# Kernel optimization log

Measured on AMD Instinct MI355X. Metric: run time of the kernel, lower is better.

The kernel has to match this reference:

```python
import jax, jax.numpy as jnp
import numpy as np

EMBED_DIM = 1024
NUM_HEADS = 16
HEAD_DIM = EMBED_DIM // NUM_HEADS
EPSILON = 0.01
C = 2.0 + EPSILON
SCORE_SCALE = 1.0
B, L = 2, 2048


def setup_inputs() -> dict:
    key = jax.random.key(0)
    k0, k1, k2, k3, k4 = jax.random.split(key, 5)
    x = jax.random.normal(k0, (B, L, EMBED_DIM), dtype=jnp.float32)
    # flax Linear kernels: (in, out)
    W_qkv = jax.random.normal(k1, (EMBED_DIM, 3 * EMBED_DIM), dtype=jnp.float32) / np.sqrt(EMBED_DIM)
    b_qkv = jnp.zeros((3 * EMBED_DIM,), dtype=jnp.float32)
    W_out = jax.random.normal(k2, (EMBED_DIM, EMBED_DIM), dtype=jnp.float32) / np.sqrt(EMBED_DIM)
    b_out = jnp.zeros((EMBED_DIM,), dtype=jnp.float32)
    return {"x": x, "W_qkv": W_qkv, "b_qkv": b_qkv, "W_out": W_out, "b_out": b_out}


def reference(x, W_qkv, b_qkv, W_out, b_out):
    Bb, Ll, E = x.shape
    qkv = x @ W_qkv + b_qkv                      # [B, L, 3E]
    q, k, v = jnp.split(qkv, 3, axis=-1)
    def to_heads(t):
        return t.reshape(Bb, Ll, NUM_HEADS, HEAD_DIM).transpose(0, 2, 1, 3)  # [B,H,L,D]
    q, k, v = to_heads(q), to_heads(k), to_heads(v)
    q_norm = q / jnp.linalg.norm(q, axis=-1, keepdims=True)
    k_norm = k / jnp.linalg.norm(k, axis=-1, keepdims=True)
    x_dot = jnp.einsum('bhid,bhjd->bhij', q_norm, k_norm)   # [B,H,L,L]
    scores = (x_dot ** 2) / (C - 2.0 * x_dot) * SCORE_SCALE
    mask = jnp.triu(jnp.ones((Ll, Ll), dtype=scores.dtype), k=1) * -1e9
    scores = scores + mask[None, None, :, :]
    attn = jax.nn.softmax(scores, axis=-1)
    out = jnp.einsum('bhij,bhjd->bhid', attn, v)            # [B,H,L,D]
    out = out.transpose(0, 2, 1, 3).reshape(Bb, Ll, E)
    return out @ W_out + b_out
```

## Files before the change

### kernel.cpp

```cpp
#include <hip/hip_runtime.h>
#include <cstdint>
#include <cstddef>

#define B_DIM 2
#define L_DIM 2048
#define E_DIM 1024
#define H_DIM 16
#define HD    64
#define M_ROWS (B_DIM * L_DIM)
#define QKV_N  (3 * E_DIM)
#define C_CONST 2.01f
#define NCH_BH 80
#define LOG2E 1.4426950408889634f
#define LN2   0.6931471805599453f

typedef unsigned short ushort_t;
typedef __attribute__((ext_vector_type(8))) short bf16x8;
typedef __attribute__((ext_vector_type(4))) float f32x4;

__device__ __forceinline__ unsigned int f2bf(float f) {
    union { float f; unsigned int u; } v; v.f = f;
    return (v.u + 0x7FFFu + ((v.u >> 16) & 1u)) >> 16;
}
__device__ __forceinline__ float bf2f_lo(unsigned int u) {
    union { unsigned int u; float f; } v; v.u = u << 16; return v.f;
}
__device__ __forceinline__ float bf2f_hi(unsigned int u) {
    union { unsigned int u; float f; } v; v.u = u & 0xffff0000u; return v.f;
}

__device__ __forceinline__ void gload16(const void* g, void* l) {
    __builtin_amdgcn_global_load_lds(
        (const __attribute__((address_space(1))) void*)g,
        (__attribute__((address_space(3))) void*)l, 16, 0, 0);
}

__global__ __launch_bounds__(256) void cast_bf16_kernel(
    const float* __restrict__ in, ushort_t* __restrict__ out, int n4)
{
    const int i = blockIdx.x * 256 + threadIdx.x;
    if (i >= n4) return;
    const float4 v = ((const float4*)in)[i];
    uint2 p;
    p.x = f2bf(v.x) | (f2bf(v.y) << 16);
    p.y = f2bf(v.z) | (f2bf(v.w) << 16);
    ((uint2*)out)[i] = p;
}

__global__ __launch_bounds__(256) void transpose_bf16_kernel(
    const float* __restrict__ in, ushort_t* __restrict__ out, int R, int Cn)
{
    __shared__ float t[64][65];
    const int c0 = blockIdx.x * 64, r0 = blockIdx.y * 64;
    const int tid = threadIdx.x;
    for (int idx = tid; idx < 4096; idx += 256) {
        const int r = idx >> 6, c = idx & 63;
        t[r][c] = in[(size_t)(r0 + r) * Cn + c0 + c];
    }
    __syncthreads();
    for (int idx = tid; idx < 4096; idx += 256) {
        const int c = idx >> 6, r = idx & 63;
        out[(size_t)(c0 + c) * R + r0 + r] = (ushort_t)f2bf(t[r][c]);
    }
}

template<int NCOLS, int MODE>
__global__ __launch_bounds__(256) void gemm_bt_kernel(
    const ushort_t* __restrict__ A, const ushort_t* __restrict__ BT,
    const float* __restrict__ bias, float* __restrict__ outf,
    ushort_t* __restrict__ q16, ushort_t* __restrict__ k16,
    ushort_t* __restrict__ v16)
{
    __shared__ __align__(16) ushort_t Abuf[128 * 32];
    __shared__ __align__(16) ushort_t Bbuf[128 * 32];
    const int tid = threadIdx.x;
    const int wave = tid >> 6, lane = tid & 63;
    const int m0 = blockIdx.x * 128, n0 = blockIdx.y * 128;
    const int wr = (wave >> 1) * 64, wc = (wave & 1) * 64;
    const int g = lane >> 4, l15 = lane & 15;

    f32x4 acc[4][4];
    #pragma unroll
    for (int i = 0; i < 4; ++i)
        #pragma unroll
        for (int j = 0; j < 4; ++j) acc[i][j] = f32x4{0.f, 0.f, 0.f, 0.f};

    const int sr = tid >> 2;
    const int sc = (tid & 3) * 8;
    const ushort_t* Asrc0 = A + (size_t)(m0 + sr) * 1024 + sc;
    const ushort_t* Asrc1 = A + (size_t)(m0 + 64 + sr) * 1024 + sc;
    const ushort_t* Bsrc0 = BT + (size_t)(n0 + sr) * 1024 + sc;
    const ushort_t* Bsrc1 = BT + (size_t)(n0 + 64 + sr) * 1024 + sc;
    ushort_t* Adst0 = &Abuf[tid * 8];
    ushort_t* Adst1 = &Abuf[2048 + tid * 8];
    ushort_t* Bdst0 = &Bbuf[tid * 8];
    ushort_t* Bdst1 = &Bbuf[2048 + tid * 8];

    for (int k0 = 0; k0 < 1024; k0 += 32) {
        __syncthreads();
        gload16(Asrc0 + k0, Adst0);
        gload16(Asrc1 + k0, Adst1);
        gload16(Bsrc0 + k0, Bdst0);
        gload16(Bsrc1 + k0, Bdst1);
        __syncthreads();

        bf16x8 af[4];
        #pragma unroll
        for (int mt = 0; mt < 4; ++mt)
            af[mt] = *(const bf16x8*)&Abuf[(wr + mt * 16 + l15) * 32 + 8 * g];
        #pragma unroll
        for (int nt = 0; nt < 4; ++nt) {
            const bf16x8 bfr = *(const bf16x8*)&Bbuf[(wc + nt * 16 + l15) * 32 + 8 * g];
            #pragma unroll
            for (int mt = 0; mt < 4; ++mt)
                acc[mt][nt] = __builtin_amdgcn_mfma_f32_16x16x32_bf16(af[mt], bfr, acc[mt][nt], 0, 0, 0);
        }
    }

    if (MODE == 0) {
        const int nBase = n0 + wc;
        const int sel = nBase >> 10;
        const int h   = (nBase & 1023) >> 6;
        float bv[4];
        #pragma unroll
        for (int nt = 0; nt < 4; ++nt) bv[nt] = bias[nBase + nt * 16 + l15];

        if (sel <= 1) {
            ushort_t* dst16 = (sel == 0) ? q16 : k16;
            #pragma unroll
            for (int mt = 0; mt < 4; ++mt) {
                float val[4][4], ss[4] = {0.f, 0.f, 0.f, 0.f};
                #pragma unroll
                for (int nt = 0; nt < 4; ++nt)
                    #pragma unroll
                    for (int r = 0; r < 4; ++r) {
                        const float v = acc[mt][nt][r] + bv[nt];
                        val[nt][r] = v;
                        ss[r] = fmaf(v, v, ss[r]);
                    }
                #pragma unroll
                for (int r = 0; r < 4; ++r) {
                    float t = ss[r];
                    t += __shfl_xor(t, 1); t += __shfl_xor(t, 2);
                    t += __shfl_xor(t, 4); t += __shfl_xor(t, 8);
                    ss[r] = 1.0f / sqrtf(t);
                }
                #pragma unroll
                for (int r = 0; r < 4; ++r) {
                    const int m = m0 + wr + mt * 16 + 4 * g + r;
                    const int bb = m >> 11, ll = m & 2047;
                    ushort_t* base = dst16 + ((size_t)((bb * H_DIM + h) * L_DIM + ll)) * HD + l15;
                    #pragma unroll
                    for (int nt = 0; nt < 4; ++nt)
                        base[nt * 16] = (ushort_t)f2bf(val[nt][r] * ss[r]);
                }
            }
        } else {
            #pragma unroll
            for (int mt = 0; mt < 4; ++mt)
                #pragma unroll
                for (int r = 0; r < 4; ++r) {
                    const int m = m0 + wr + mt * 16 + 4 * g + r;
                    const int bb = m >> 11, ll = m & 2047;
                    ushort_t* base = v16 + ((size_t)((bb * H_DIM + h) * L_DIM + ll)) * HD + l15;
                    #pragma unroll
                    for (int nt = 0; nt < 4; ++nt)
                        base[nt * 16] = (ushort_t)f2bf(acc[mt][nt][r] + bv[nt]);
                }
        }
    } else {
        #pragma unroll
        for (int nt = 0; nt < 4; ++nt) {
            const int n = n0 + wc + nt * 16 + l15;
            const float bvv = bias[n];
            #pragma unroll
            for (int mt = 0; mt < 4; ++mt)
                #pragma unroll
                for (int r = 0; r < 4; ++r) {
                    const int m = m0 + wr + mt * 16 + 4 * g + r;
                    outf[(size_t)m * E_DIM + n] = acc[mt][nt][r] + bvv;
                }
        }
    }
}

__global__ __launch_bounds__(256) void vt_transpose_kernel(
    const ushort_t* __restrict__ vb, ushort_t* __restrict__ vt)
{
    __shared__ ushort_t t[64][68];
    const int kt = blockIdx.x, bh = blockIdx.y;
    const int tid = threadIdx.x;
    const ushort_t* src = vb + ((size_t)bh * L_DIM + kt * 64) * HD;
    #pragma unroll
    for (int p = 0; p < 16; ++p) {
        const int idx = tid + 256 * p;
        t[idx >> 6][idx & 63] = src[idx];
    }
    __syncthreads();
    ushort_t* dst = vt + (size_t)bh * HD * L_DIM + kt * 64;
    #pragma unroll
    for (int p = 0; p < 16; ++p) {
        const int idx = tid + 256 * p;
        const int d = idx >> 6, k = idx & 63;
        dst[(size_t)d * L_DIM + k] = t[k][d];
    }
}

__global__ __launch_bounds__(256) void attn_mfma_kernel(
    const ushort_t* __restrict__ qn, const ushort_t* __restrict__ kn,
    const ushort_t* __restrict__ vt,
    ushort_t* __restrict__ pO, float* __restrict__ pl, float* __restrict__ pm)
{
    __shared__ __align__(16) ushort_t Qs[64 * 64];
    __shared__ __align__(16) ushort_t Ks[2][64 * 64];
    __shared__ __align__(16) ushort_t Vs[2][64 * 64];

    int c = blockIdx.x, qt = 0, s = 0;
    #pragma unroll
    for (int gg = 0; gg < 4; ++gg) {
        const int sz = 8 * (gg + 1);
        if (c < sz) { qt = 8 * gg + c / (gg + 1); s = c - (c / (gg + 1)) * (gg + 1); break; }
        c -= sz;
    }
    const int bh = blockIdx.y;
    const int cid = bh * NCH_BH + blockIdx.x;
    const int q0 = qt * 64;
    const int kt0 = 8 * s;
    const int ktEnd = min(8 * s + 8, qt + 1);

    const int tid = threadIdx.x, w = tid >> 6, lane = tid & 63;
    const int g = lane >> 4, l15 = lane & 15;
    ushort_t* Pw = &Qs[w * 16 * 64];

    const ushort_t* Qg = qn + ((size_t)bh * L_DIM + q0) * HD;
    const ushort_t* Kg = kn + (size_t)bh * L_DIM * HD;
    const ushort_t* Vg = vt + (size_t)bh * HD * L_DIM;

    const int srow = tid >> 3, sch = tid & 7;
    const int srow2 = (tid + 256) >> 3, sch2 = (tid + 256) & 7;

    {
        const int j0 = kt0 * 64;
        gload16(Qg + srow * 64 + ((sch ^ (srow & 7)) << 3), Qs + srow * 64 + (sch << 3));
        gload16(Qg + srow2 * 64 + ((sch2 ^ (srow2 & 7)) << 3), Qs + srow2 * 64 + (sch2 << 3));
        gload16(Kg + (size_t)(j0 + srow) * 64 + ((sch ^ (srow & 7)) << 3), Ks[0] + srow * 64 + (sch << 3));
        gload16(Kg + (size_t)(j0 + srow2) * 64 + ((sch2 ^ (srow2 & 7)) << 3), Ks[0] + srow2 * 64 + (sch2 << 3));
        gload16(Vg + (size_t)srow * L_DIM + j0 + ((sch ^ (srow & 7)) << 3), Vs[0] + srow * 64 + (sch << 3));
        gload16(Vg + (size_t)srow2 * L_DIM + j0 + ((sch2 ^ (srow2 & 7)) << 3), Vs[0] + srow2 * 64 + (sch2 << 3));
    }
    __syncthreads();

    bf16x8 qf[2];
    #pragma unroll
    for (int kc = 0; kc < 2; ++kc) {
        const int row = 16 * w + l15;
        qf[kc] = *(const bf16x8*)&Qs[row * 64 + (((4 * kc + g) ^ (row & 7)) << 3)];
    }

    f32x4 o[4];
    float M = 8.0f * LOG2E, l_i = 0.f;
    #pragma unroll
    for (int j = 0; j < 4; ++j) o[j] = f32x4{0.f, 0.f, 0.f, 0.f};

    const int qrow = q0 + 16 * w + l15;

    for (int kt = kt0; kt < ktEnd; ++kt) {
        const int cur = (kt - kt0) & 1;
        if (kt + 1 < ktEnd) {
            const int j1 = (kt + 1) * 64;
            gload16(Kg + (size_t)(j1 + srow) * 64 + ((sch ^ (srow & 7)) << 3),
                    Ks[cur ^ 1] + srow * 64 + (sch << 3));
            gload16(Kg + (size_t)(j1 + srow2) * 64 + ((sch2 ^ (srow2 & 7)) << 3),
                    Ks[cur ^ 1] + srow2 * 64 + (sch2 << 3));
            gload16(Vg + (size_t)srow * L_DIM + j1 + ((sch ^ (srow & 7)) << 3),
                    Vs[cur ^ 1] + srow * 64 + (sch << 3));
            gload16(Vg + (size_t)srow2 * L_DIM + j1 + ((sch2 ^ (srow2 & 7)) << 3),
                    Vs[cur ^ 1] + srow2 * 64 + (sch2 << 3));
        }
        const int j0 = kt * 64;

        bf16x8 ak[4][2];
        #pragma unroll
        for (int kt4 = 0; kt4 < 4; ++kt4)
            #pragma unroll
            for (int kc = 0; kc < 2; ++kc) {
                const int row = 16 * kt4 + l15;
                ak[kt4][kc] = *(const bf16x8*)&Ks[cur][row * 64 + (((4 * kc + g) ^ (row & 7)) << 3)];
            }
        f32x4 st[4];
        #pragma unroll
        for (int kt4 = 0; kt4 < 4; ++kt4) st[kt4] = f32x4{0.f, 0.f, 0.f, 0.f};
        __builtin_amdgcn_s_setprio(1);
        #pragma unroll
        for (int kc = 0; kc < 2; ++kc)
            #pragma unroll
            for (int kt4 = 0; kt4 < 4; ++kt4)
                st[kt4] = __builtin_amdgcn_mfma_f32_16x16x32_bf16(
                    ak[kt4][kc], qf[kc], st[kt4], 0, 0, 0);
        __builtin_amdgcn_s_setprio(0);

        const float negM = -M;
        float emax = -1e30f;
        #pragma unroll
        for (int kt4 = 0; kt4 < 4; ++kt4)
            #pragma unroll
            for (int r = 0; r < 4; ++r) {
                const float x = st[kt4][r];
                const float t = (x * x) * LOG2E;
                const float d = fmaf(-2.f, x, C_CONST);
                float rr;
                asm("v_rcp_f32 %0, %1" : "=v"(rr) : "v"(d));
                const float e = fmaf(t, rr, negM);
                st[kt4][r] = e;
                emax = fmaxf(emax, e);
            }

        if (kt == qt) {
            emax = -1e30f;
            #pragma unroll
            for (int kt4 = 0; kt4 < 4; ++kt4)
                #pragma unroll
                for (int r = 0; r < 4; ++r) {
                    const int key = j0 + 16 * kt4 + 4 * g + r;
                    float e = st[kt4][r];
                    e = (key > qrow) ? -100.f : e;
                    st[kt4][r] = e;
                    emax = fmaxf(emax, e);
                }
        }

        if (__any(emax > 0.f)) {
            float rm = fmaxf(emax, __shfl_xor(emax, 16));
            rm = fmaxf(rm, __shfl_xor(rm, 32));
            rm = fmaxf(rm, 0.f);
            #pragma unroll
            for (int kt4 = 0; kt4 < 4; ++kt4)
                #pragma unroll
                for (int r = 0; r < 4; ++r) st[kt4][r] -= rm;
            const float nrm = -rm;
            float scl;
            asm("v_exp_f32 %0, %1" : "=v"(scl) : "v"(nrm));
            l_i *= scl;
            #pragma unroll
            for (int r = 0; r < 4; ++r) {
                const float sv = __shfl(scl, 4 * g + r);
                #pragma unroll
                for (int dt = 0; dt < 4; ++dt) o[dt][r] *= sv;
            }
            M += rm;
        }

        float ts = 0.f;
        #pragma unroll
        for (int kt4 = 0; kt4 < 4; ++kt4) {
            const float e0 = st[kt4][0], e1 = st[kt4][1];
            const float e2 = st[kt4][2], e3 = st[kt4][3];
            float p0, p1, p2, p3;
            asm("v_exp_f32 %0, %1" : "=v"(p0) : "v"(e0));
            asm("v_exp_f32 %0, %1" : "=v"(p1) : "v"(e1));
            asm("v_exp_f32 %0, %1" : "=v"(p2) : "v"(e2));
            asm("v_exp_f32 %0, %1" : "=v"(p3) : "v"(e3));
            ts += (p0 + p1) + (p2 + p3);
            uint2 pk;
            asm("v_cvt_pk_bf16_f32 %0, %1, %2" : "=v"(pk.x) : "v"(p0), "v"(p1));
            asm("v_cvt_pk_bf16_f32 %0, %1, %2" : "=v"(pk.y) : "v"(p2), "v"(p3));
            const int ch = 2 * kt4 + (g >> 1);
            *(uint2*)&Pw[l15 * 64 + ((ch ^ (l15 & 7)) << 3) + 4 * (g & 1)] = pk;
        }
        l_i += ts;

        bf16x8 ap[2], av[4][2];
        #pragma unroll
        for (int kc = 0; kc < 2; ++kc)
            ap[kc] = *(const bf16x8*)&Pw[l15 * 64 + (((4 * kc + g) ^ (l15 & 7)) << 3)];
        #pragma unroll
        for (int dt = 0; dt < 4; ++dt)
            #pragma unroll
            for (int kc = 0; kc < 2; ++kc) {
                const int row = 16 * dt + l15;
                av[dt][kc] = *(const bf16x8*)&Vs[cur][row * 64 + (((4 * kc + g) ^ (row & 7)) << 3)];
            }
        __builtin_amdgcn_s_setprio(1);
        #pragma unroll
        for (int kc = 0; kc < 2; ++kc)
            #pragma unroll
            for (int dt = 0; dt < 4; ++dt)
                o[dt] = __builtin_amdgcn_mfma_f32_16x16x32_bf16(
                    ap[kc], av[dt][kc], o[dt], 0, 0, 0);
        __builtin_amdgcn_s_setprio(0);

        __syncthreads();
    }

    l_i += __shfl_xor(l_i, 16);
    l_i += __shfl_xor(l_i, 32);
    ushort_t* po = pO + (size_t)cid * 4096 + (16 * w) * 64;
    #pragma unroll
    for (int r = 0; r < 4; ++r)
        #pragma unroll
        for (int dt = 0; dt < 4; ++dt)
            po[(4 * g + r) * 64 + 16 * dt + l15] = (ushort_t)f2bf(o[dt][r]);
    if (lane < 16) {
        pl[cid * 64 + 16 * w + lane] = l_i;
        pm[cid * 64 + 16 * w + lane] = M * LN2;
    }
}

__global__ __launch_bounds__(256) void combine_kernel(
    const ushort_t* __restrict__ pO, const float* __restrict__ pl,
    const float* __restrict__ pm, ushort_t* __restrict__ cb)
{
    const int qt = blockIdx.x, bh = blockIdx.y;
    const int gg = qt >> 3, ns = gg + 1;
    const int cid0 = bh * NCH_BH + 4 * gg * (gg + 1) + (qt & 7) * (gg + 1);
    const int tid = threadIdx.x;
    const int row = tid >> 2, seg = tid & 3;

    float mt = -1e30f;
    for (int s2 = 0; s2 < ns; ++s2)
        mt = fmaxf(mt, pm[(cid0 + s2) * 64 + row]);

    float acc[16];
    #pragma unroll
    for (int j = 0; j < 16; ++j) acc[j] = 0.f;
    float l_tot = 0.f;
    for (int s2 = 0; s2 < ns; ++s2) {
        const int cid = cid0 + s2;
        const float sc = __expf(pm[cid * 64 + row] - mt);
        l_tot += pl[cid * 64 + row] * sc;
        const ushort_t* src = pO + (size_t)cid * 4096 + row * 64 + seg * 16;
        const uint4 u0 = *(const uint4*)src;
        const uint4 u1 = *(const uint4*)(src + 8);
        const unsigned int uu[8] = {u0.x, u0.y, u0.z, u0.w, u1.x, u1.y, u1.z, u1.w};
        #pragma unroll
        for (int j = 0; j < 8; ++j) {
            acc[2 * j]     = fmaf(sc, bf2f_lo(uu[j]), acc[2 * j]);
            acc[2 * j + 1] = fmaf(sc, bf2f_hi(uu[j]), acc[2 * j + 1]);
        }
    }
    const float inv = 1.0f / l_tot;
    const int b = bh >> 4, h = bh & 15;
    ushort_t* dst = cb + ((size_t)(b * L_DIM + qt * 64 + row)) * E_DIM + h * HD + seg * 16;
    uint4 w0, w1;
    w0.x = f2bf(acc[0] * inv)  | (f2bf(acc[1] * inv) << 16);
    w0.y = f2bf(acc[2] * inv)  | (f2bf(acc[3] * inv) << 16);
    w0.z = f2bf(acc[4] * inv)  | (f2bf(acc[5] * inv) << 16);
    w0.w = f2bf(acc[6] * inv)  | (f2bf(acc[7] * inv) << 16);
    w1.x = f2bf(acc[8] * inv)  | (f2bf(acc[9] * inv) << 16);
    w1.y = f2bf(acc[10] * inv) | (f2bf(acc[11] * inv) << 16);
    w1.z = f2bf(acc[12] * inv) | (f2bf(acc[13] * inv) << 16);
    w1.w = f2bf(acc[14] * inv) | (f2bf(acc[15] * inv) << 16);
    *(uint4*)dst = w0;
    *(uint4*)(dst + 8) = w1;
}

extern "C" void kernel_launch(void* const* d_in, const int* in_sizes, int n_in,
                              void* d_out, int out_size, void* d_ws, size_t ws_size,
                              hipStream_t stream)
{
    const float* x    = (const float*)d_in[0];
    const float* Wqkv = (const float*)d_in[1];
    const float* bqkv = (const float*)d_in[2];
    const float* Wout = (const float*)d_in[3];
    const float* bout = (const float*)d_in[4];
    float* out = (float*)d_out;

    char* ws = (char*)d_ws;
    const size_t MB = 1u << 20;
    ushort_t* qn16  = (ushort_t*)(ws + 0 * MB);
    ushort_t* kn16  = (ushort_t*)(ws + 8 * MB);
    ushort_t* vb16  = (ushort_t*)(ws + 16 * MB);
    ushort_t* vt16  = (ushort_t*)(ws + 24 * MB);
    ushort_t* xb    = (ushort_t*)(ws + 32 * MB);
    ushort_t* cb    = (ushort_t*)(ws + 32 * MB);
    ushort_t* WqkvT = (ushort_t*)(ws + 40 * MB);
    ushort_t* pO    = (ushort_t*)(ws + 40 * MB);
    float*    pl    = (float*)   (ws + 60 * MB);
    float*    pm    = (float*)   (ws + 61 * MB);
    ushort_t* WoutT = (ushort_t*)(ws + 62 * MB);

    cast_bf16_kernel<<<4096, 256, 0, stream>>>(x, xb, (M_ROWS * E_DIM) / 4);
    transpose_bf16_kernel<<<dim3(QKV_N / 64, E_DIM / 64), 256, 0, stream>>>(Wqkv, WqkvT, E_DIM, QKV_N);

    gemm_bt_kernel<QKV_N, 0><<<dim3(M_ROWS / 128, QKV_N / 128), 256, 0, stream>>>(
        xb, WqkvT, bqkv, nullptr, qn16, kn16, vb16);

    vt_transpose_kernel<<<dim3(L_DIM / 64, B_DIM * H_DIM), 256, 0, stream>>>(vb16, vt16);

    transpose_bf16_kernel<<<dim3(E_DIM / 64, E_DIM / 64), 256, 0, stream>>>(Wout, WoutT, E_DIM, E_DIM);

    attn_mfma_kernel<<<dim3(NCH_BH, B_DIM * H_DIM), 256, 0, stream>>>(qn16, kn16, vt16, pO, pl, pm);

    combine_kernel<<<dim3(L_DIM / 64, B_DIM * H_DIM), 256, 0, stream>>>(pO, pl, pm, cb);

    gemm_bt_kernel<E_DIM, 1><<<dim3(M_ROWS / 128, E_DIM / 128), 256, 0, stream>>>(
        cb, WoutT, bout, out, nullptr, nullptr, nullptr);
}
```

Measured before the change: 129.7 us.

## Use 128-row query tiles in attention and merge prep kernels into one launch

The attention kernel now processes 128 query rows per block with 8 waves (512 threads), so each K/V tile loaded into shared memory serves twice as many queries. This halves the number of split chunks per head and the K/V reload traffic. The causal mask is applied to the last two key tiles. Separately, the x cast and both weight transposes are fused into a single prep kernel, saving two launches. The risks are more idle work on the diagonal for the larger query tile, fewer blocks for load balancing, and higher per-block LDS use.

```diff
diff --git a/kernel.cpp b/kernel.cpp
--- a/kernel.cpp
+++ b/kernel.cpp
@@ -10,7 +10,7 @@
 #define M_ROWS (B_DIM * L_DIM)
 #define QKV_N  (3 * E_DIM)
 #define C_CONST 2.01f
-#define NCH_BH 80
+#define NCH_BH 40
 #define LOG2E 1.4426950408889634f
 #define LN2   0.6931471805599453f
 
@@ -35,24 +35,10 @@
         (__attribute__((address_space(3))) void*)l, 16, 0, 0);
 }
 
-__global__ __launch_bounds__(256) void cast_bf16_kernel(
-    const float* __restrict__ in, ushort_t* __restrict__ out, int n4)
-{
-    const int i = blockIdx.x * 256 + threadIdx.x;
-    if (i >= n4) return;
-    const float4 v = ((const float4*)in)[i];
-    uint2 p;
-    p.x = f2bf(v.x) | (f2bf(v.y) << 16);
-    p.y = f2bf(v.z) | (f2bf(v.w) << 16);
-    ((uint2*)out)[i] = p;
-}
-
-__global__ __launch_bounds__(256) void transpose_bf16_kernel(
-    const float* __restrict__ in, ushort_t* __restrict__ out, int R, int Cn)
-{
-    __shared__ float t[64][65];
-    const int c0 = blockIdx.x * 64, r0 = blockIdx.y * 64;
-    const int tid = threadIdx.x;
+__device__ __forceinline__ void transpose_tile_dev(
+    const float* __restrict__ in, ushort_t* __restrict__ out,
+    int R, int Cn, int c0, int r0, int tid, float t[64][65])
+{
     for (int idx = tid; idx < 4096; idx += 256) {
         const int r = idx >> 6, c = idx & 63;
         t[r][c] = in[(size_t)(r0 + r) * Cn + c0 + c];
@@ -61,6 +47,30 @@
     for (int idx = tid; idx < 4096; idx += 256) {
         const int c = idx >> 6, r = idx & 63;
         out[(size_t)(c0 + c) * R + r0 + r] = (ushort_t)f2bf(t[r][c]);
+    }
+}
+
+__global__ __launch_bounds__(256) void prep_kernel(
+    const float* __restrict__ x, ushort_t* __restrict__ xb,
+    const float* __restrict__ Wqkv, ushort_t* __restrict__ WqkvT,
+    const float* __restrict__ Wout, ushort_t* __restrict__ WoutT)
+{
+    __shared__ float t[64][65];
+    const int bx = blockIdx.x;
+    const int tid = threadIdx.x;
+    if (bx < 4096) {
+        const int i = bx * 256 + tid;
+        const float4 v = ((const float4*)x)[i];
+        uint2 p;
+        p.x = f2bf(v.x) | (f2bf(v.y) << 16);
+        p.y = f2bf(v.z) | (f2bf(v.w) << 16);
+        ((uint2*)xb)[i] = p;
+    } else if (bx < 4096 + 768) {
+        const int idx = bx - 4096;
+        transpose_tile_dev(Wqkv, WqkvT, E_DIM, QKV_N, (idx % 48) * 64, (idx / 48) * 64, tid, t);
+    } else {
+        const int idx = bx - 4864;
+        transpose_tile_dev(Wout, WoutT, E_DIM, E_DIM, (idx & 15) * 64, (idx >> 4) * 64, tid, t);
     }
 }
 
@@ -206,27 +216,27 @@
     }
 }
 
-__global__ __launch_bounds__(256) void attn_mfma_kernel(
+__global__ __launch_bounds__(512) void attn_mfma_kernel(
     const ushort_t* __restrict__ qn, const ushort_t* __restrict__ kn,
     const ushort_t* __restrict__ vt,
     ushort_t* __restrict__ pO, float* __restrict__ pl, float* __restrict__ pm)
 {
-    __shared__ __align__(16) ushort_t Qs[64 * 64];
+    __shared__ __align__(16) ushort_t Qs[128 * 64];
     __shared__ __align__(16) ushort_t Ks[2][64 * 64];
     __shared__ __align__(16) ushort_t Vs[2][64 * 64];
 
-    int c = blockIdx.x, qt = 0, s = 0;
+    int c = blockIdx.x, qtp = 0, s = 0;
     #pragma unroll
     for (int gg = 0; gg < 4; ++gg) {
-        const int sz = 8 * (gg + 1);
-        if (c < sz) { qt = 8 * gg + c / (gg + 1); s = c - (c / (gg + 1)) * (gg + 1); break; }
+        const int sz = 4 * (gg + 1);
+        if (c < sz) { qtp = 4 * gg + c / (gg + 1); s = c - (c / (gg + 1)) * (gg + 1); break; }
         c -= sz;
     }
     const int bh = blockIdx.y;
     const int cid = bh * NCH_BH + blockIdx.x;
-    const int q0 = qt * 64;
+    const int q0 = qtp * 128;
     const int kt0 = 8 * s;
-    const int ktEnd = min(8 * s + 8, qt + 1);
+    const int ktEnd = min(8 * s + 8, 2 * qtp + 2);
 
     const int tid = threadIdx.x, w = tid >> 6, lane = tid & 63;
     const int g = lane >> 4, l15 = lane & 15;
@@ -237,16 +247,14 @@
     const ushort_t* Vg = vt + (size_t)bh * HD * L_DIM;
 
     const int srow = tid >> 3, sch = tid & 7;
-    const int srow2 = (tid + 256) >> 3, sch2 = (tid + 256) & 7;
+    const int qr2 = (tid + 512) >> 3, qc2 = (tid + 512) & 7;
 
     {
         const int j0 = kt0 * 64;
         gload16(Qg + srow * 64 + ((sch ^ (srow & 7)) << 3), Qs + srow * 64 + (sch << 3));
-        gload16(Qg + srow2 * 64 + ((sch2 ^ (srow2 & 7)) << 3), Qs + srow2 * 64 + (sch2 << 3));
+        gload16(Qg + qr2 * 64 + ((qc2 ^ (qr2 & 7)) << 3), Qs + qr2 * 64 + (qc2 << 3));
         gload16(Kg + (size_t)(j0 + srow) * 64 + ((sch ^ (srow & 7)) << 3), Ks[0] + srow * 64 + (sch << 3));
-        gload16(Kg + (size_t)(j0 + srow2) * 64 + ((sch2 ^ (srow2 & 7)) << 3), Ks[0] + srow2 * 64 + (sch2 << 3));
         gload16(Vg + (size_t)srow * L_DIM + j0 + ((sch ^ (srow & 7)) << 3), Vs[0] + srow * 64 + (sch << 3));
-        gload16(Vg + (size_t)srow2 * L_DIM + j0 + ((sch2 ^ (srow2 & 7)) << 3), Vs[0] + srow2 * 64 + (sch2 << 3));
     }
     __syncthreads();
 
@@ -270,12 +278,8 @@
             const int j1 = (kt + 1) * 64;
             gload16(Kg + (size_t)(j1 + srow) * 64 + ((sch ^ (srow & 7)) << 3),
                     Ks[cur ^ 1] + srow * 64 + (sch << 3));
-            gload16(Kg + (size_t)(j1 + srow2) * 64 + ((sch2 ^ (srow2 & 7)) << 3),
-                    Ks[cur ^ 1] + srow2 * 64 + (sch2 << 3));
             gload16(Vg + (size_t)srow * L_DIM + j1 + ((sch ^ (srow & 7)) << 3),
                     Vs[cur ^ 1] + srow * 64 + (sch << 3));
-            gload16(Vg + (size_t)srow2 * L_DIM + j1 + ((sch2 ^ (srow2 & 7)) << 3),
-                    Vs[cur ^ 1] + srow2 * 64 + (sch2 << 3));
         }
         const int j0 = kt * 64;
 
@@ -315,7 +319,7 @@
                 emax = fmaxf(emax, e);
             }
 
-        if (kt == qt) {
+        if (kt >= 2 * qtp) {
             emax = -1e30f;
             #pragma unroll
             for (int kt4 = 0; kt4 < 4; ++kt4)
@@ -394,15 +398,15 @@
 
     l_i += __shfl_xor(l_i, 16);
     l_i += __shfl_xor(l_i, 32);
-    ushort_t* po = pO + (size_t)cid * 4096 + (16 * w) * 64;
+    ushort_t* po = pO + (size_t)cid * 8192 + (16 * w) * 64;
     #pragma unroll
     for (int r = 0; r < 4; ++r)
         #pragma unroll
         for (int dt = 0; dt < 4; ++dt)
             po[(4 * g + r) * 64 + 16 * dt + l15] = (ushort_t)f2bf(o[dt][r]);
     if (lane < 16) {
-        pl[cid * 64 + 16 * w + lane] = l_i;
-        pm[cid * 64 + 16 * w + lane] = M * LN2;
+        pl[cid * 128 + 16 * w + lane] = l_i;
+        pm[cid * 128 + 16 * w + lane] = M * LN2;
     }
 }
 
@@ -410,15 +414,17 @@
     const ushort_t* __restrict__ pO, const float* __restrict__ pl,
     const float* __restrict__ pm, ushort_t* __restrict__ cb)
 {
-    const int qt = blockIdx.x, bh = blockIdx.y;
-    const int gg = qt >> 3, ns = gg + 1;
-    const int cid0 = bh * NCH_BH + 4 * gg * (gg + 1) + (qt & 7) * (gg + 1);
+    const int qt2 = blockIdx.x, bh = blockIdx.y;
+    const int qtp = qt2 >> 1, half = qt2 & 1;
+    const int gg = qtp >> 2, ns = gg + 1;
+    const int cid0 = bh * NCH_BH + 2 * gg * (gg + 1) + (qtp & 3) * ns;
     const int tid = threadIdx.x;
     const int row = tid >> 2, seg = tid & 3;
+    const int rowc = half * 64 + row;
 
     float mt = -1e30f;
     for (int s2 = 0; s2 < ns; ++s2)
-        mt = fmaxf(mt, pm[(cid0 + s2) * 64 + row]);
+        mt = fmaxf(mt, pm[(cid0 + s2) * 128 + rowc]);
 
     float acc[16];
     #pragma unroll
@@ -426,9 +432,9 @@
     float l_tot = 0.f;
     for (int s2 = 0; s2 < ns; ++s2) {
         const int cid = cid0 + s2;
-        const float sc = __expf(pm[cid * 64 + row] - mt);
-        l_tot += pl[cid * 64 + row] * sc;
-        const ushort_t* src = pO + (size_t)cid * 4096 + row * 64 + seg * 16;
+        const float sc = __expf(pm[cid * 128 + rowc] - mt);
+        l_tot += pl[cid * 128 + rowc] * sc;
+        const ushort_t* src = pO + (size_t)cid * 8192 + rowc * 64 + seg * 16;
         const uint4 u0 = *(const uint4*)src;
         const uint4 u1 = *(const uint4*)(src + 8);
         const unsigned int uu[8] = {u0.x, u0.y, u0.z, u0.w, u1.x, u1.y, u1.z, u1.w};
@@ -440,7 +446,7 @@
     }
     const float inv = 1.0f / l_tot;
     const int b = bh >> 4, h = bh & 15;
-    ushort_t* dst = cb + ((size_t)(b * L_DIM + qt * 64 + row)) * E_DIM + h * HD + seg * 16;
+    ushort_t* dst = cb + ((size_t)(b * L_DIM + qt2 * 64 + row)) * E_DIM + h * HD + seg * 16;
     uint4 w0, w1;
     w0.x = f2bf(acc[0] * inv)  | (f2bf(acc[1] * inv) << 16);
     w0.y = f2bf(acc[2] * inv)  | (f2bf(acc[3] * inv) << 16);
@@ -479,17 +485,14 @@
     float*    pm    = (float*)   (ws + 61 * MB);
     ushort_t* WoutT = (ushort_t*)(ws + 62 * MB);
 
-    cast_bf16_kernel<<<4096, 256, 0, stream>>>(x, xb, (M_ROWS * E_DIM) / 4);
-    transpose_bf16_kernel<<<dim3(QKV_N / 64, E_DIM / 64), 256, 0, stream>>>(Wqkv, WqkvT, E_DIM, QKV_N);
+    prep_kernel<<<5120, 256, 0, stream>>>(x, xb, Wqkv, WqkvT, Wout, WoutT);
 
     gemm_bt_kernel<QKV_N, 0><<<dim3(M_ROWS / 128, QKV_N / 128), 256, 0, stream>>>(
         xb, WqkvT, bqkv, nullptr, qn16, kn16, vb16);
 
     vt_transpose_kernel<<<dim3(L_DIM / 64, B_DIM * H_DIM), 256, 0, stream>>>(vb16, vt16);
 
-    transpose_bf16_kernel<<<dim3(E_DIM / 64, E_DIM / 64), 256, 0, stream>>>(Wout, WoutT, E_DIM, E_DIM);
-
-    attn_mfma_kernel<<<dim3(NCH_BH, B_DIM * H_DIM), 256, 0, stream>>>(qn16, kn16, vt16, pO, pl, pm);
+    attn_mfma_kernel<<<dim3(NCH_BH, B_DIM * H_DIM), 512, 0, stream>>>(qn16, kn16, vt16, pO, pl, pm);
 
     combine_kernel<<<dim3(L_DIM / 64, B_DIM * H_DIM), 256, 0, stream>>>(pO, pl, pm, cb);
 
```

Result: faster. 122.8 us (-5.3%).
